# Optimization experiments

Hardware: AMD Instinct MI355X
Metric: run time of the kernel (lower is better)

Reference implementation:

```python
import jax, jax.numpy as jnp
import numpy as np

GROUPS = 8
EPS = 1e-3  # keras GroupNormalization default epsilon


def group_norm(x, gamma, beta):
    # x: [B,H,W,C], groups over channel axis
    B, H, W, C = x.shape
    g = GROUPS
    xr = x.reshape(B, H, W, g, C // g)
    mean = jnp.mean(xr, axis=(1, 2, 4), keepdims=True)
    var = jnp.var(xr, axis=(1, 2, 4), keepdims=True)
    xn = (xr - mean) * jax.lax.rsqrt(var + EPS)
    xn = xn.reshape(B, H, W, C)
    return xn * gamma + beta


def setup_inputs() -> dict:
    key = jax.random.key(0)
    ks = jax.random.split(key, 6)
    B, H, W, C = 8, 64, 64, 64
    std = 0.02
    return {
        "x": jax.random.normal(ks[0], (B, H, W, C), dtype=jnp.float32),
        "gamma": jnp.ones((C,), dtype=jnp.float32),
        "beta": jnp.zeros((C,), dtype=jnp.float32),
        "wq": jax.random.normal(ks[1], (C, C), dtype=jnp.float32) * std,
        "bq": jnp.zeros((C,), dtype=jnp.float32),
        "wk": jax.random.normal(ks[2], (C, C), dtype=jnp.float32) * std,
        "bk": jnp.zeros((C,), dtype=jnp.float32),
        "wv": jax.random.normal(ks[3], (C, C), dtype=jnp.float32) * std,
        "bv": jnp.zeros((C,), dtype=jnp.float32),
        "wp": jax.random.normal(ks[4], (C, C), dtype=jnp.float32) * std,
        "bp": jnp.zeros((C,), dtype=jnp.float32),
    }


def reference(x, gamma, beta, wq, bq, wk, bk, wv, bv, wp, bp):
    B, H, W, C = x.shape
    scale = jnp.asarray(C, x.dtype) ** -0.5
    h = group_norm(x, gamma, beta)  # note: residual uses normalized input (as in source)
    q = h @ wq + bq
    k = h @ wk + bk
    v = h @ wv + bv
    # full O((HW)^2) score tensor, exactly as the original
    attn = jnp.einsum('bhwc,bHWc->bhwHW', q, k) * scale
    attn = jax.nn.softmax(attn.reshape(B, H, W, H * W), axis=-1)
    attn = attn.reshape(B, H, W, H, W)
    proj = jnp.einsum('bhwHW,bHWc->bhwc', attn, v)
    proj = proj @ wp + bp
    return h + proj
```

## Files before the change

### kernel.cpp

```cpp
#include <hip/hip_runtime.h>

#define NTOK 4096
#define CH 64
#define LOG2E 1.4426950408889634f

typedef __bf16 bf8 __attribute__((ext_vector_type(8)));
typedef __bf16 bf4 __attribute__((ext_vector_type(4)));
typedef _Float16 h8 __attribute__((ext_vector_type(8)));
typedef _Float16 h4 __attribute__((ext_vector_type(4)));
typedef float f4 __attribute__((ext_vector_type(4)));

__device__ __forceinline__ f4 mfma16(bf8 a, bf8 b, f4 c) {
    return __builtin_amdgcn_mfma_f32_16x16x32_bf16(a, b, c, 0, 0, 0);
}
__device__ __forceinline__ f4 mfma16h(h4 a, h4 b, f4 c) {
    return __builtin_amdgcn_mfma_f32_16x16x16f16(a, b, c, 0, 0, 0);
}

__global__ __launch_bounds__(256) void pre_kernel(const float* __restrict__ wq,
                                                  const float* __restrict__ wk,
                                                  const float* __restrict__ wv,
                                                  const float* __restrict__ wp,
                                                  const float* __restrict__ x,
                                                  __bf16* __restrict__ wqt,
                                                  __bf16* __restrict__ wkt,
                                                  __bf16* __restrict__ wvt,
                                                  __bf16* __restrict__ wpt,
                                                  float* __restrict__ gpart) {
    int t = threadIdx.x;
    if (blockIdx.x < 4) {
        int m = blockIdx.x;
        const float* src = (m == 0) ? wq : (m == 1) ? wk : (m == 2) ? wv : wp;
        __bf16* dst      = (m == 0) ? wqt : (m == 1) ? wkt : (m == 2) ? wvt : wpt;
        __shared__ float s[64][65];
        for (int i = 0; i < 16; ++i) {
            int e = i * 256 + t;
            s[e >> 6][e & 63] = src[e];
        }
        __syncthreads();
        int o = t >> 2, seg = t & 3;
        for (int j = 0; j < 16; ++j) {
            int in = seg * 16 + j;
            dst[o * 64 + in] = (__bf16)s[in][o];
        }
        return;
    }
    int bid = blockIdx.x - 4;
    int b = bid >> 6, slab = bid & 63;
    const float4* xb = (const float4*)(x + (size_t)(b * NTOK + slab * 64) * CH);
    float s = 0.f, ss = 0.f;
    for (int i = 0; i < 4; ++i) {
        int row = (t >> 4) + i * 16;
        float4 v = xb[row * 16 + (t & 15)];
        s  += v.x + v.y + v.z + v.w;
        ss += v.x * v.x + v.y * v.y + v.z * v.z + v.w * v.w;
    }
    __shared__ float ls[256], lss[256];
    ls[t] = s; lss[t] = ss;
    __syncthreads();
    if (t < 8) {
        float a = 0.f, aa = 0.f;
        for (int p = 0; p < 16; ++p) {
            a  += ls[p * 16 + 2 * t]  + ls[p * 16 + 2 * t + 1];
            aa += lss[p * 16 + 2 * t] + lss[p * 16 + 2 * t + 1];
        }
        gpart[((b * 64 + slab) * 8 + t) * 2 + 0] = a;
        gpart[((b * 64 + slab) * 8 + t) * 2 + 1] = aa;
    }
}

__global__ __launch_bounds__(256) void qkv_gn(const float* __restrict__ x,
                                              const float* __restrict__ gpart,
                                              const float* __restrict__ gamma,
                                              const float* __restrict__ beta,
                                              const __bf16* __restrict__ wqt,
                                              const __bf16* __restrict__ wkt,
                                              const __bf16* __restrict__ wvt,
                                              const float* __restrict__ bq,
                                              const float* __restrict__ bk,
                                              const float* __restrict__ bv,
                                              __bf16* __restrict__ q,
                                              __bf16* __restrict__ k,
                                              _Float16* __restrict__ vT) {
    __shared__ __bf16 W[3][64][72];
    __shared__ __bf16 Hl[64][72];
    __shared__ _Float16 Vst[64][68];
    __shared__ float red[128];
    __shared__ float sstat[16];
    int t = threadIdx.x;
    size_t rowbase = (size_t)blockIdx.x * 64;
    int b = (int)(rowbase >> 12), tokbase = (int)(rowbase & 4095);
    if (t < 64) {
        int gi = t & 7, c = t >> 3;
        const float2* gp = (const float2*)gpart + (size_t)b * 512 + gi;
        float a = 0.f, aa = 0.f;
        for (int p = c * 8; p < c * 8 + 8; ++p) {
            float2 v = gp[(size_t)p * 8];
            a += v.x; aa += v.y;
        }
        red[t * 2] = a; red[t * 2 + 1] = aa;
    }
    for (int m = 0; m < 3; ++m) {
        const __bf16* src = (m == 0) ? wqt : (m == 1) ? wkt : wvt;
        for (int i = 0; i < 2; ++i) {
            int e = i * 256 + t, row = e >> 3, ch = e & 7;
            *(bf8*)&W[m][row][ch * 8] = *(const bf8*)(src + row * 64 + ch * 8);
        }
    }
    __syncthreads();
    if (t < 8) {
        float a = 0.f, aa = 0.f;
        for (int c = 0; c < 8; ++c) {
            a  += red[(c * 8 + t) * 2];
            aa += red[(c * 8 + t) * 2 + 1];
        }
        float mean = a * (1.f / 32768.f);
        float var = aa * (1.f / 32768.f) - mean * mean;
        sstat[t * 2 + 0] = mean;
        sstat[t * 2 + 1] = rsqrtf(var + 1e-3f);
    }
    __syncthreads();
    {
        int c4 = (t & 15) * 4, grp = c4 >> 3;
        float mean = sstat[grp * 2], rstd = sstat[grp * 2 + 1];
        float g0 = gamma[c4] * rstd, g1 = gamma[c4 + 1] * rstd,
              g2 = gamma[c4 + 2] * rstd, g3 = gamma[c4 + 3] * rstd;
        float b0 = beta[c4], b1 = beta[c4 + 1], b2 = beta[c4 + 2], b3 = beta[c4 + 3];
        const float4* xb = (const float4*)(x + rowbase * 64);
        for (int i = 0; i < 4; ++i) {
            int row = (t >> 4) + i * 16;
            float4 v = xb[row * 16 + (t & 15)];
            bf4 hv;
            hv[0] = (__bf16)((v.x - mean) * g0 + b0);
            hv[1] = (__bf16)((v.y - mean) * g1 + b1);
            hv[2] = (__bf16)((v.z - mean) * g2 + b2);
            hv[3] = (__bf16)((v.w - mean) * g3 + b3);
            *(bf4*)&Hl[row][c4] = hv;
        }
    }
    __syncthreads();
    int lane = t & 63, wave = t >> 6, quad = lane >> 4, l15 = lane & 15;
    bf8 a0 = *(const bf8*)&Hl[wave * 16 + l15][quad * 8];
    bf8 a1 = *(const bf8*)&Hl[wave * 16 + l15][32 + quad * 8];
    for (int m = 0; m < 3; ++m) {
        const float* bias = (m == 0) ? bq : (m == 1) ? bk : bv;
        float sc = (m == 0) ? 0.125f * LOG2E : 1.0f;
        for (int tt = 0; tt < 4; ++tt) {
            int col = l15 + 16 * tt;
            bf8 b0 = *(const bf8*)&W[m][col][quad * 8];
            bf8 b1 = *(const bf8*)&W[m][col][32 + quad * 8];
            f4 acc = {0.f, 0.f, 0.f, 0.f};
            acc = mfma16(a0, b0, acc);
            acc = mfma16(a1, b1, acc);
            float bb = bias[col];
            if (m == 2) {
                for (int r = 0; r < 4; ++r)
                    Vst[col][wave * 16 + quad * 4 + r] = (_Float16)(acc[r] + bb);
            } else {
                __bf16* dst = (m == 0) ? q : k;
                for (int r = 0; r < 4; ++r) {
                    float val = (acc[r] + bb) * sc;
                    dst[(rowbase + wave * 16 + quad * 4 + r) * 64 + col] = (__bf16)val;
                }
            }
        }
    }
    __syncthreads();
    {
        int d = t >> 2, seg = t & 3;
        int ktile = (tokbase >> 4) + seg;
        int p = d >> 5, u = (d >> 4) & 1, dl = d & 15;
        _Float16* base = vT + (size_t)b * 262144 + (size_t)ktile * 1024 + p * 512 + u * 4;
        for (int q4 = 0; q4 < 4; ++q4) {
            h4 c = *(const h4*)&Vst[d][seg * 16 + q4 * 4];
            *(h4*)(base + (q4 * 16 + dl) * 8) = c;
        }
    }
}

__global__ __launch_bounds__(256, 2) void attn_final(const __bf16* __restrict__ q,
                                                     const __bf16* __restrict__ k,
                                                     const _Float16* __restrict__ vt,
                                                     const __bf16* __restrict__ wpt,
                                                     const float* __restrict__ bp,
                                                     const float* __restrict__ x,
                                                     const float* __restrict__ gpart,
                                                     const float* __restrict__ gamma,
                                                     const float* __restrict__ beta,
                                                     float* __restrict__ out) {
    __shared__ _Float16 Om[2][64][72];
    __shared__ float sS[2][64];
    __shared__ __bf16 Wl[64][72];
    __shared__ __bf16 Ol[64][72];
    __shared__ float red[128];
    __shared__ float sstat[16], sg[64], sb[64];

    int bid = blockIdx.x;
    int qt = bid >> 3, b = bid & 7;
    int t = threadIdx.x, lane = t & 63, w = t >> 6, quad = lane >> 4, l15 = lane & 15;

    for (int i = 0; i < 2; ++i) {
        int e = i * 256 + t, row = e >> 3, ch = e & 7;
        *(bf8*)&Wl[row][ch * 8] = *(const bf8*)(wpt + row * 64 + ch * 8);
    }
    if (t < 64) { sg[t] = gamma[t]; sb[t] = beta[t]; }
    if (t < 64) {
        int gi = t & 7, c = t >> 3;
        const float2* gp = (const float2*)gpart + (size_t)b * 512 + gi;
        float a = 0.f, aa = 0.f;
        for (int p = c * 8; p < c * 8 + 8; ++p) {
            float2 v = gp[(size_t)p * 8];
            a += v.x; aa += v.y;
        }
        red[t * 2] = a; red[t * 2 + 1] = aa;
    }

    const __bf16* qbase = q + ((size_t)b * NTOK + qt * 64) * 64;
    bf8 aq[4][2];
    for (int s = 0; s < 4; ++s) {
        const __bf16* r = qbase + (s * 16 + l15) * 64;
        aq[s][0] = *(const bf8*)(r + quad * 8);
        aq[s][1] = *(const bf8*)(r + 32 + quad * 8);
    }
    const __bf16* kr = k + ((size_t)b * NTOK + w * 1024 + l15) * 64;
    const _Float16* vr = vt + (size_t)b * 262144 + (size_t)(w * 64) * 1024 + lane * 8;

    f4 acc[4][4] = {};
    float li[4] = {0.f, 0.f, 0.f, 0.f};

    bf8 kf0 = *(const bf8*)(kr + quad * 8);
    bf8 kf1 = *(const bf8*)(kr + 32 + quad * 8);
    h8 va = *(const h8*)(vr);
    h8 vb = *(const h8*)(vr + 512);

    #pragma unroll 1
    for (int it = 0; it < 64; ++it) {
        int nx = (it + 1) & 63;
        const __bf16* krn = kr + (size_t)nx * 1024;
        const _Float16* vrn = vr + (size_t)nx * 1024;
        bf8 nk0 = *(const bf8*)(krn + quad * 8);
        bf8 nk1 = *(const bf8*)(krn + 32 + quad * 8);
        h8 nva = *(const h8*)(vrn);
        h8 nvb = *(const h8*)(vrn + 512);

        h4 vf0 = {va[0], va[1], va[2], va[3]};
        h4 vf1 = {va[4], va[5], va[6], va[7]};
        h4 vf2 = {vb[0], vb[1], vb[2], vb[3]};
        h4 vf3 = {vb[4], vb[5], vb[6], vb[7]};

        for (int s = 0; s < 4; ++s) {
            f4 St = {0.f, 0.f, 0.f, 0.f};
            St = mfma16(kf0, aq[s][0], St);
            St = mfma16(kf1, aq[s][1], St);
            h4 pf;
            for (int r = 0; r < 4; ++r) {
                float pv = __builtin_amdgcn_exp2f(St[r]);
                li[s] += pv;
                pf[r] = (_Float16)pv;
            }
            acc[s][0] = mfma16h(vf0, pf, acc[s][0]);
            acc[s][1] = mfma16h(vf1, pf, acc[s][1]);
            acc[s][2] = mfma16h(vf2, pf, acc[s][2]);
            acc[s][3] = mfma16h(vf3, pf, acc[s][3]);
        }
        kf0 = nk0; kf1 = nk1;
        va = nva; vb = nvb;
    }

    for (int s = 0; s < 4; ++s) {
        li[s] += __shfl_xor(li[s], 16);
        li[s] += __shfl_xor(li[s], 32);
    }

    if (w >= 2) {
        for (int s = 0; s < 4; ++s) {
            for (int td = 0; td < 4; ++td) {
                h4 o4;
                for (int r = 0; r < 4; ++r) o4[r] = (_Float16)acc[s][td][r];
                *(h4*)&Om[w - 2][s * 16 + l15][td * 16 + quad * 4] = o4;
            }
            if (quad == 0) sS[w - 2][s * 16 + l15] = li[s];
        }
    }
    __syncthreads();
    if (t < 8) {
        float a = 0.f, aa = 0.f;
        for (int c = 0; c < 8; ++c) {
            a  += red[(c * 8 + t) * 2];
            aa += red[(c * 8 + t) * 2 + 1];
        }
        float mean = a * (1.f / 32768.f);
        float var = aa * (1.f / 32768.f) - mean * mean;
        sstat[t * 2 + 0] = mean;
        sstat[t * 2 + 1] = rsqrtf(var + 1e-3f);
    }
    if (w < 2) {
        for (int s = 0; s < 4; ++s) {
            for (int td = 0; td < 4; ++td) {
                h4 o4 = *(const h4*)&Om[w][s * 16 + l15][td * 16 + quad * 4];
                for (int r = 0; r < 4; ++r) acc[s][td][r] += (float)o4[r];
            }
            li[s] += sS[w][s * 16 + l15];
        }
    }
    __syncthreads();
    if (w < 2) {
        for (int s = 0; s < 4; ++s) {
            for (int td = 0; td < 4; ++td) {
                h4 o4;
                for (int r = 0; r < 4; ++r) o4[r] = (_Float16)acc[s][td][r];
                *(h4*)&Om[w][s * 16 + l15][td * 16 + quad * 4] = o4;
            }
            if (quad == 0) sS[w][s * 16 + l15] = li[s];
        }
    }
    __syncthreads();
    {
        int qq = t >> 2, ds = (t & 3) * 16;
        float inv = 1.f / (sS[0][qq] + sS[1][qq]);
        h8 a0 = *(const h8*)&Om[0][qq][ds];
        h8 b0 = *(const h8*)&Om[0][qq][ds + 8];
        h8 a1 = *(const h8*)&Om[1][qq][ds];
        h8 b1 = *(const h8*)&Om[1][qq][ds + 8];
        bf8 olo, ohi;
        for (int j = 0; j < 8; ++j) {
            olo[j] = (__bf16)(((float)a0[j] + (float)a1[j]) * inv);
            ohi[j] = (__bf16)(((float)b0[j] + (float)b1[j]) * inv);
        }
        *(bf8*)&Ol[qq][ds] = olo;
        *(bf8*)&Ol[qq][ds + 8] = ohi;
    }
    __syncthreads();
    size_t rowbase = ((size_t)b * NTOK + qt * 64) + w * 16;
    bf8 a0 = *(const bf8*)&Ol[w * 16 + l15][quad * 8];
    bf8 a1 = *(const bf8*)&Ol[w * 16 + l15][32 + quad * 8];
    for (int tt = 0; tt < 4; ++tt) {
        int col = l15 + 16 * tt;
        bf8 b0 = *(const bf8*)&Wl[col][quad * 8];
        bf8 b1 = *(const bf8*)&Wl[col][32 + quad * 8];
        f4 pacc = {0.f, 0.f, 0.f, 0.f};
        pacc = mfma16(a0, b0, pacc);
        pacc = mfma16(a1, b1, pacc);
        int grp = col >> 3;
        float mean = sstat[grp * 2], gs = sg[col] * sstat[grp * 2 + 1], bs = sb[col];
        float bias = bp[col];
        for (int r = 0; r < 4; ++r) {
            size_t gi = (rowbase + quad * 4 + r) * 64 + col;
            float h = (x[gi] - mean) * gs + bs;
            out[gi] = pacc[r] + bias + h;
        }
    }
}

extern "C" void kernel_launch(void* const* d_in, const int* in_sizes, int n_in,
                              void* d_out, int out_size, void* d_ws, size_t ws_size,
                              hipStream_t stream) {
    const float* x     = (const float*)d_in[0];
    const float* gamma = (const float*)d_in[1];
    const float* beta  = (const float*)d_in[2];
    const float* wq    = (const float*)d_in[3];
    const float* bq    = (const float*)d_in[4];
    const float* wk    = (const float*)d_in[5];
    const float* bk    = (const float*)d_in[6];
    const float* wv    = (const float*)d_in[7];
    const float* bv    = (const float*)d_in[8];
    const float* wp    = (const float*)d_in[9];
    const float* bp    = (const float*)d_in[10];
    float* out = (float*)d_out;

    char* ws = (char*)d_ws;
    const size_t MB = 1024 * 1024;
    __bf16*   qb   = (__bf16*)(ws);
    __bf16*   kb   = (__bf16*)(ws + 4 * MB);
    _Float16* vtb  = (_Float16*)(ws + 8 * MB);
    __bf16*   wqt  = (__bf16*)(ws + 12 * MB);
    __bf16*   wkt  = (__bf16*)(ws + 12 * MB + 8192);
    __bf16*   wvt  = (__bf16*)(ws + 12 * MB + 16384);
    __bf16*   wpt  = (__bf16*)(ws + 12 * MB + 24576);
    float*    gpart = (float*)(ws + 12 * MB + 32768);

    pre_kernel<<<516, 256, 0, stream>>>(wq, wk, wv, wp, x, wqt, wkt, wvt, wpt, gpart);
    qkv_gn<<<512, 256, 0, stream>>>(x, gpart, gamma, beta, wqt, wkt, wvt, bq, bk, bv, qb, kb, vtb);
    attn_final<<<512, 256, 0, stream>>>(qb, kb, vtb, wpt, bp, x, gpart, gamma, beta, out);
}
```

Before: 136.4 us.

## Use 16x16x32 f16 MFMA for PV with 32-key steps and new V layout

Switches the P·V product from the 16x16x16 f16 MFMA to the 16x16x32 f16 MFMA, so each iteration handles 32 keys and the number of PV instructions is halved. The V transpose written in the projection kernel is reorganised so each lane loads a contiguous 8-element fragment matching the new operand layout. The explicit next-iteration register prefetch of K/V is dropped in favour of a simpler loop with half as many iterations, which may expose load latency unless the compiler schedules the loads early.

```diff
diff --git a/kernel.cpp b/kernel.cpp
--- a/kernel.cpp
+++ b/kernel.cpp
@@ -13,8 +13,8 @@
 __device__ __forceinline__ f4 mfma16(bf8 a, bf8 b, f4 c) {
     return __builtin_amdgcn_mfma_f32_16x16x32_bf16(a, b, c, 0, 0, 0);
 }
-__device__ __forceinline__ f4 mfma16h(h4 a, h4 b, f4 c) {
-    return __builtin_amdgcn_mfma_f32_16x16x16f16(a, b, c, 0, 0, 0);
+__device__ __forceinline__ f4 mfma32h(h8 a, h8 b, f4 c) {
+    return __builtin_amdgcn_mfma_f32_16x16x32_f16(a, b, c, 0, 0, 0);
 }
 
 __global__ __launch_bounds__(256) void pre_kernel(const float* __restrict__ wq,
@@ -167,13 +167,16 @@
     }
     __syncthreads();
     {
-        int d = t >> 2, seg = t & 3;
-        int ktile = (tokbase >> 4) + seg;
-        int p = d >> 5, u = (d >> 4) & 1, dl = d & 15;
-        _Float16* base = vT + (size_t)b * 262144 + (size_t)ktile * 1024 + p * 512 + u * 4;
-        for (int q4 = 0; q4 < 4; ++q4) {
-            h4 c = *(const h4*)&Vst[d][seg * 16 + q4 * 4];
-            *(h4*)(base + (q4 * 16 + dl) * 8) = c;
+        int d = wave * 16 + l15;
+        for (int kb = 0; kb < 2; ++kb) {
+            h4 lo = *(const h4*)&Vst[d][kb * 32 + quad * 4];
+            h4 hi = *(const h4*)&Vst[d][kb * 32 + 16 + quad * 4];
+            h8 o;
+            o[0] = lo[0]; o[1] = lo[1]; o[2] = lo[2]; o[3] = lo[3];
+            o[4] = hi[0]; o[5] = hi[1]; o[6] = hi[2]; o[7] = hi[3];
+            _Float16* dst = vT + ((((size_t)b * 128 + (tokbase >> 5) + kb) * 4 + wave) * 64
+                                  + lane) * 8;
+            *(h8*)dst = o;
         }
     }
 }
@@ -222,49 +225,47 @@
         aq[s][0] = *(const bf8*)(r + quad * 8);
         aq[s][1] = *(const bf8*)(r + 32 + quad * 8);
     }
-    const __bf16* kr = k + ((size_t)b * NTOK + w * 1024 + l15) * 64;
-    const _Float16* vr = vt + (size_t)b * 262144 + (size_t)(w * 64) * 1024 + lane * 8;
+    const __bf16* kbase   = k  + ((size_t)b * NTOK + w * 1024) * 64;
+    const _Float16* vbase = vt + (size_t)b * 262144 + (size_t)(w * 32) * 2048 + lane * 8;
 
     f4 acc[4][4] = {};
     float li[4] = {0.f, 0.f, 0.f, 0.f};
 
-    bf8 kf0 = *(const bf8*)(kr + quad * 8);
-    bf8 kf1 = *(const bf8*)(kr + 32 + quad * 8);
-    h8 va = *(const h8*)(vr);
-    h8 vb = *(const h8*)(vr + 512);
-
-    #pragma unroll 1
-    for (int it = 0; it < 64; ++it) {
-        int nx = (it + 1) & 63;
-        const __bf16* krn = kr + (size_t)nx * 1024;
-        const _Float16* vrn = vr + (size_t)nx * 1024;
-        bf8 nk0 = *(const bf8*)(krn + quad * 8);
-        bf8 nk1 = *(const bf8*)(krn + 32 + quad * 8);
-        h8 nva = *(const h8*)(vrn);
-        h8 nvb = *(const h8*)(vrn + 512);
-
-        h4 vf0 = {va[0], va[1], va[2], va[3]};
-        h4 vf1 = {va[4], va[5], va[6], va[7]};
-        h4 vf2 = {vb[0], vb[1], vb[2], vb[3]};
-        h4 vf3 = {vb[4], vb[5], vb[6], vb[7]};
+    for (int it = 0; it < 32; ++it) {
+        const __bf16* kr0 = kbase + (size_t)(it * 32 + l15) * 64;
+        const __bf16* kr1 = kr0 + 16 * 64;
+        bf8 kf00 = *(const bf8*)(kr0 + quad * 8);
+        bf8 kf01 = *(const bf8*)(kr0 + 32 + quad * 8);
+        bf8 kf10 = *(const bf8*)(kr1 + quad * 8);
+        bf8 kf11 = *(const bf8*)(kr1 + 32 + quad * 8);
+        const _Float16* vr = vbase + (size_t)it * 2048;
+        h8 vf0 = *(const h8*)(vr);
+        h8 vf1 = *(const h8*)(vr + 512);
+        h8 vf2 = *(const h8*)(vr + 1024);
+        h8 vf3 = *(const h8*)(vr + 1536);
 
         for (int s = 0; s < 4; ++s) {
-            f4 St = {0.f, 0.f, 0.f, 0.f};
-            St = mfma16(kf0, aq[s][0], St);
-            St = mfma16(kf1, aq[s][1], St);
-            h4 pf;
+            f4 St0 = {0.f, 0.f, 0.f, 0.f};
+            f4 St1 = {0.f, 0.f, 0.f, 0.f};
+            St0 = mfma16(kf00, aq[s][0], St0);
+            St0 = mfma16(kf01, aq[s][1], St0);
+            St1 = mfma16(kf10, aq[s][0], St1);
+            St1 = mfma16(kf11, aq[s][1], St1);
+            h8 pf;
+            float rs = 0.f;
             for (int r = 0; r < 4; ++r) {
-                float pv = __builtin_amdgcn_exp2f(St[r]);
-                li[s] += pv;
-                pf[r] = (_Float16)pv;
-            }
-            acc[s][0] = mfma16h(vf0, pf, acc[s][0]);
-            acc[s][1] = mfma16h(vf1, pf, acc[s][1]);
-            acc[s][2] = mfma16h(vf2, pf, acc[s][2]);
-            acc[s][3] = mfma16h(vf3, pf, acc[s][3]);
-        }
-        kf0 = nk0; kf1 = nk1;
-        va = nva; vb = nvb;
+                float p0 = __builtin_amdgcn_exp2f(St0[r]);
+                float p1 = __builtin_amdgcn_exp2f(St1[r]);
+                rs += p0 + p1;
+                pf[r]     = (_Float16)p0;
+                pf[4 + r] = (_Float16)p1;
+            }
+            li[s] += rs;
+            acc[s][0] = mfma32h(vf0, pf, acc[s][0]);
+            acc[s][1] = mfma32h(vf1, pf, acc[s][1]);
+            acc[s][2] = mfma32h(vf2, pf, acc[s][2]);
+            acc[s][3] = mfma32h(vf3, pf, acc[s][3]);
+        }
     }
 
     for (int s = 0; s < 4; ++s) {
```

After: 133.3 us. 1.02x faster.
